# Kernel tuning notes

Hardware: AMD Instinct MI355X
Metric: run time of the kernel (lower is better)

## Reference

```python
import jax, jax.numpy as jnp
import numpy as np

ALPHA = 0.25
GAMMA = 2.0
LAMBDA_T = 0.1


def count_components(fg):
    """Count 6-connected components per volume. fg: [M,H,W,D] bool.
    Min-label propagation + pointer jumping (parallel union-find style CCL),
    matching scipy.ndimage.label's default face-connectivity structure.
    Returns float32 [M] component counts."""
    M, H, W, D = fg.shape
    N = H * W * D
    BIG = jnp.int32(N)  # sentinel label for background / padding
    idx = jnp.arange(N, dtype=jnp.int32).reshape(1, H, W, D)
    L0 = jnp.broadcast_to(idx, fg.shape)

    def shift(a, axis, d):
        # b[i] = a[i-d] along `axis`, padded with BIG outside the volume
        pad = [(0, 0)] * 4
        pad[axis] = (max(d, 0), max(-d, 0))
        ap = jnp.pad(a, pad, constant_values=N)
        sl = [slice(None)] * 4
        sl[axis] = slice(max(-d, 0), max(-d, 0) + a.shape[axis])
        return ap[tuple(sl)]

    def one_step(L):
        Lv = jnp.where(fg, L, BIG)
        m = Lv
        for ax in (1, 2, 3):
            for d in (1, -1):
                m = jnp.minimum(m, shift(Lv, ax, d))
        Ln = jnpp_min = jnp.where(fg, jnp.minimum(L, m), L)
        # pointer jumping (L <- L[L]) twice for log-depth convergence
        Lf = Ln.reshape(M, N)
        Lf = jnp.take_along_axis(Lf, Lf, axis=1)
        Lf = jnp.take_along_axis(Lf, Lf, axis=1)
        return Lf.reshape(M, H, W, D)

    def cond(s):
        return s[1]

    def body(s):
        L, _ = s
        Ln = one_step(L)
        return (Ln, jnp.any(Ln != L))

    L, _ = jax.lax.while_loop(cond, body, (L0, jnp.bool_(True)))
    # at fixed point every foreground component carries its min linear index;
    # roots satisfy L[i] == i
    roots = fg & (L == idx)
    return jnp.sum(roots, axis=(1, 2, 3)).astype(jnp.float32)


def _focal(x, t):
    p = jax.nn.sigmoid(x)
    pt = jnp.where(t == 1, p, 1.0 - p)
    bce = jax.nn.softplus(x) - x * t  # BCE-with-logits, elementwise
    alpha_t = jnp.where(t == 1, ALPHA, 1.0 - ALPHA)
    return jnp.mean(alpha_t * (1.0 - pt) ** GAMMA * bce)


def _topology(x, t):
    B, C = x.shape[:2]
    spatial = x.shape[2:]
    fg_p = (jax.nn.sigmoid(x) > 0.5).reshape(B * C, *spatial)
    fg_t = (t > 0.5).reshape(B * C, *spatial)
    cc_p = count_components(fg_p).reshape(B, C).mean(axis=0)  # mean over batch per class
    cc_t = count_components(fg_t).reshape(B, C).mean(axis=0)
    return jnp.mean(jnp.abs(cc_p - cc_t))  # sum over classes / C


def setup_inputs() -> dict:
    key = jax.random.key(0)
    k1, k2 = jax.random.split(key)
    shape = (2, 2, 96, 96, 96)
    pred_logits = jax.random.normal(k1, shape, dtype=jnp.float32)
    target_binary = jax.random.randint(k2, shape, 0, 2).astype(jnp.float32)
    return {"pred_logits": pred_logits, "target_binary": target_binary}


def reference(pred_logits, target_binary):
    focal = _focal(pred_logits, target_binary)
    topo = jax.lax.stop_gradient(_topology(pred_logits, target_binary))
    return focal + LAMBDA_T * topo
```

## Files before the change

kernel.cpp:

```cpp
#include <hip/hip_runtime.h>
#include <math.h>

#define N_VOX (96*96*96)
#define NVOL 8
#define NEL (4*N_VOX)
#define PLANE (96*96)

#define TW 8
#define TH 8
#define TILES_W 12
#define TILES_H 12
#define TILE_VOX (96*TW*TH)
#define TILE_WORDS (TILE_VOX/32)

#define NBPLANES 11
#define NPAIRS (2*NBPLANES)
#define FACES_PER_VOL (2*NPAIRS*PLANE)
#define MAXR 40192
#define FALLR 65536
#define SEGCAP 4608
#define HT2N 4096
#define MAX_PROBES 16

#define WS_ACC   0
#define WS_ROOT  256
#define WS_EVT   1536
#define WS_PCNT  2816
#define WS_HDR   4096

__device__ __forceinline__ int uf_find(int* __restrict__ L, int x) {
    int r = x;
    int p = L[r];
    while (p != r) { r = p; p = L[r]; }
    if (r != x) atomicMin(&L[x], r);
    return r;
}

__device__ __forceinline__ int uf_merge(int* __restrict__ L, int l1, int l2) {
    int ev = 0;
    while (l1 != l2) {
        if (l1 < l2) { int t = l1; l1 = l2; l2 = t; }
        int l3 = atomicMin(&L[l1], l2);
        if (l3 == l1) { ev++; l1 = l2; }
        else l1 = l3;
    }
    return ev;
}

__device__ __forceinline__ void merge_local(int* lab, int l1, int l2) {
    while (l1 != l2 && l1 != lab[l1]) l1 = lab[l1];
    while (l1 != l2 && l2 != lab[l2]) l2 = lab[l2];
    while (l1 != l2) {
        if (l1 < l2) { int t = l1; l1 = l2; l2 = t; }
        int l3 = atomicMin(&lab[l1], l2);
        l1 = (l3 == l1) ? l2 : l3;
    }
}

__device__ __forceinline__ int run_start(const unsigned* fm, int i, int d) {
    int rowb = (i - d) >> 5;
    int k = d >> 5, bit = d & 31;
    unsigned below = bit ? (~fm[rowb + k] & ((1u << bit) - 1)) : 0u;
    int z = -1;
    if (below) z = (k << 5) + 31 - __builtin_clz(below);
    else if (k > 0) {
        unsigned n1 = ~fm[rowb + k - 1];
        if (n1) z = ((k - 1) << 5) + 31 - __builtin_clz(n1);
        else if (k > 1) {
            unsigned n0 = ~fm[rowb];
            if (n0) z = 31 - __builtin_clz(n0);
        }
    }
    return (i - d) + z + 1;
}

__global__ __launch_bounds__(256) void ccl_local(const float* __restrict__ pred,
                                                 const float* __restrict__ targ,
                                                 unsigned short* __restrict__ faces,
                                                 int* __restrict__ rootcnt,
                                                 float* __restrict__ acc,
                                                 int vbase) {
    __shared__ int lab[TILE_VOX];
    __shared__ unsigned fm[TILE_WORDS];
    __shared__ float fws[4];
    __shared__ int   iws[4];
    __shared__ int   gbase;

    int vloc = blockIdx.y;
    int v = vbase + vloc;
    int tile = blockIdx.x;
    int tw = tile % TILES_W, th = tile / TILES_W;
    int w0 = tw * TW, h0 = th * TH;
    int tbase = h0 * PLANE + w0 * 96;
    unsigned short* Fw = faces + (size_t)vloc * FACES_PER_VOL;
    unsigned short* Fh = Fw + 2 * NBPLANES * PLANE;

    float fsum = 0.0f;
    for (int it = 0; it < TILE_VOX / 256; it++) {
        int i = it * 256 + threadIdx.x;
        int lh = i / 768;
        int j = tbase + i + lh * 8448;
        bool f;
        if (v < 4) {
            float xv = pred[(size_t)v * N_VOX + j];
            float tv = targ[(size_t)v * N_VOX + j];
            f = xv > 0.0f;
            float m   = (tv == 1.0f) ? -xv : xv;
            float at  = (tv == 1.0f) ? 0.25f : 0.75f;
            float e   = __expf(-fabsf(m));
            float inv = 1.0f / (1.0f + e);
            float sig = inv * ((m >= 0.0f) ? 1.0f : e);
            float sp  = fmaxf(m, 0.0f) + __logf(1.0f + e);
            fsum += at * sig * sig * sp;
        } else {
            f = targ[(size_t)(v - 4) * N_VOX + j] > 0.5f;
        }
        unsigned long long bal = __ballot(f);
        if ((threadIdx.x & 63) == 0) {
            fm[i >> 5]       = (unsigned)bal;
            fm[(i >> 5) + 1] = (unsigned)(bal >> 32);
        }
        lab[i] = i;
    }
    __syncthreads();

    for (int t = threadIdx.x; t < 336; t += 256) {
        bool wdir = t < 168;
        int tt = wdir ? t : t - 168;
        int lh, lw, k;
        if (wdir) { lh = tt / 21; int rem = tt % 21; lw = rem / 3; k = rem % 3; }
        else      { lh = tt / 24; int rem = tt % 24; lw = rem / 3; k = rem % 3; }
        int wb = (lh * 8 + lw) * 3 + k;
        int nb = wb + (wdir ? 3 : 24);
        unsigned ov = fm[wb] & fm[nb];
        if (!ov) continue;
        unsigned carry = (k > 0) ? ((fm[wb - 1] & fm[nb - 1]) >> 31) : 0u;
        unsigned starts = ov & ~((ov << 1) | carry);
        int base_i = wb << 5;
        int dir = wdir ? 96 : 768;
        while (starts) {
            int b = __builtin_ctz(starts);
            starts &= starts - 1;
            int i = base_i + b;
            int d = (k << 5) + b;
            merge_local(lab, run_start(fm, i, d), run_start(fm, i + dir, d));
        }
    }
    __syncthreads();

    int myroots = 0;
    for (int t = threadIdx.x; t < TILE_WORDS; t += 256) {
        unsigned m = fm[t];
        if (!m) continue;
        unsigned carry = (t % 3) ? (fm[t - 1] >> 31) : 0u;
        unsigned starts = m & ~((m << 1) | carry);
        int base_i = t << 5;
        while (starts) {
            int b = __builtin_ctz(starts); starts &= starts - 1;
            if (lab[base_i + b] == base_i + b) myroots++;
        }
    }
    int s = myroots;
    for (int off = 1; off < 64; off <<= 1) {
        int tv2 = __shfl_up(s, off, 64);
        if ((threadIdx.x & 63) >= off) s += tv2;
    }
    int wid = threadIdx.x >> 6;
    if ((threadIdx.x & 63) == 63) iws[wid] = s;
    __syncthreads();
    int wbase = 0;
    for (int k = 0; k < wid; k++) wbase += iws[k];
    if (threadIdx.x == 0)
        gbase = atomicAdd(&rootcnt[v << 5], iws[0] + iws[1] + iws[2] + iws[3]);
    __syncthreads();
    int nid = gbase + wbase + (s - myroots);

    for (int t = threadIdx.x; t < TILE_WORDS; t += 256) {
        unsigned m = fm[t];
        if (!m) continue;
        unsigned carry = (t % 3) ? (fm[t - 1] >> 31) : 0u;
        unsigned starts = m & ~((m << 1) | carry);
        int base_i = t << 5;
        while (starts) {
            int b = __builtin_ctz(starts); starts &= starts - 1;
            int i = base_i + b;
            if (lab[i] == i) lab[i] = ~(nid++);
        }
    }
    __syncthreads();

    for (int t = threadIdx.x; t < TILE_WORDS; t += 256) {
        unsigned m = fm[t];
        if (!m) continue;
        unsigned carry = (t % 3) ? (fm[t - 1] >> 31) : 0u;
        unsigned starts = m & ~((m << 1) | carry);
        int base_i = t << 5;
        while (starts) {
            int b = __builtin_ctz(starts); starts &= starts - 1;
            int i = base_i + b;
            int p = lab[i];
            if (p >= 0) {
                int r = p, q2 = lab[r];
                while (q2 >= 0) { r = q2; q2 = lab[r]; }
                lab[i] = q2;
            }
        }
    }
    __syncthreads();

    for (int t = threadIdx.x; t < 768; t += 256) {
        int f  = t / 192;
        int g  = t % 192;
        int u  = g / 24;
        int d4 = (g % 24) * 4;
        int i0; unsigned short* dst;
        if (f == 0) {
            if (tw == 0) continue;
            i0  = u * 768 + d4;
            dst = Fw + ((tw - 1) * 2 + 1) * PLANE + (h0 + u) * 96 + d4;
        } else if (f == 1) {
            if (tw == TILES_W - 1) continue;
            i0  = u * 768 + 7 * 96 + d4;
            dst = Fw + (tw * 2) * PLANE + (h0 + u) * 96 + d4;
        } else if (f == 2) {
            if (th == 0) continue;
            i0  = u * 96 + d4;
            dst = Fh + ((th - 1) * 2 + 1) * PLANE + (w0 + u) * 96 + d4;
        } else {
            if (th == TILES_H - 1) continue;
            i0  = 7 * 768 + u * 96 + d4;
            dst = Fh + (th * 2) * PLANE + (w0 + u) * 96 + d4;
        }
        unsigned mw = fm[i0 >> 5];
        unsigned short vals[4];
        bool prevf = false;
        for (int q = 0; q < 4; q++) {
            bool fb = (mw >> ((d4 & 31) + q)) & 1;
            if (fb) vals[q] = prevf ? vals[q - 1]
                                    : (unsigned short)(~lab[run_start(fm, i0 + q, d4 + q)]);
            else vals[q] = 0xFFFFu;
            prevf = fb;
        }
        *(ushort4*)dst = make_ushort4(vals[0], vals[1], vals[2], vals[3]);
    }

    for (int off = 32; off; off >>= 1) fsum += __shfl_down(fsum, off, 64);
    if ((threadIdx.x & 63) == 0) fws[wid] = fsum;
    __syncthreads();
    if (threadIdx.x == 0) {
        float ft = fws[0] + fws[1] + fws[2] + fws[3];
        if (v < 4 && ft != 0.0f) atomicAdd(acc, ft);
    }
}

__global__ __launch_bounds__(256) void ccl_pairs(const unsigned short* __restrict__ faces,
                                                 unsigned* __restrict__ pairs,
                                                 int* __restrict__ pcnt,
                                                 int vbase) {
    __shared__ unsigned ht[HT2N];
    __shared__ int nloc;
    for (int i = threadIdx.x; i < HT2N; i += 256) ht[i] = 0xFFFFFFFFu;
    if (threadIdx.x == 0) nloc = 0;
    __syncthreads();

    int f    = blockIdx.x;
    int vloc = blockIdx.y;
    int v    = vbase + vloc;
    const unsigned short* A = faces + (size_t)vloc * FACES_PER_VOL
                                    + (size_t)(2 * f) * PLANE;
    const unsigned short* B = A + PLANE;
    unsigned* pb = pairs + ((size_t)vloc * NPAIRS + f) * SEGCAP;

    const int GPP = PLANE / 8;
    for (int g = threadIdx.x; g < GPP; g += 256) {
        int e8 = g * 8;
        int4 aw = *(const int4*)(A + e8);
        int4 bw = *(const int4*)(B + e8);
        unsigned a32[4] = {(unsigned)aw.x, (unsigned)aw.y, (unsigned)aw.z, (unsigned)aw.w};
        unsigned b32[4] = {(unsigned)bw.x, (unsigned)bw.y, (unsigned)bw.z, (unsigned)bw.w};
        bool pf = false;
        if (e8 % 96) pf = (A[e8 - 1] != 0xFFFFu) && (B[e8 - 1] != 0xFFFFu);
        #pragma unroll
        for (int q = 0; q < 8; q++) {
            unsigned av = (a32[q >> 1] >> ((q & 1) * 16)) & 0xFFFFu;
            unsigned bv = (b32[q >> 1] >> ((q & 1) * 16)) & 0xFFFFu;
            bool f2 = (av != 0xFFFFu) && (bv != 0xFFFFu);
            if (f2 && !pf && av != bv) {
                unsigned lo = av < bv ? av : bv;
                unsigned hi = av < bv ? bv : av;
                unsigned key = (lo << 16) | hi;
                unsigned h = (key * 2654435761u) >> 20;
                bool fresh = false;
                for (int pr = 0; pr < MAX_PROBES; pr++) {
                    unsigned prev = atomicCAS(&ht[h], 0xFFFFFFFFu, key);
                    if (prev == 0xFFFFFFFFu) { fresh = true; break; }
                    if (prev == key) break;
                    h = (h + 1) & (HT2N - 1);
                    if (pr == MAX_PROBES - 1) fresh = true;
                }
                if (fresh) {
                    int ix = atomicAdd(&nloc, 1);
                    pb[ix] = key;
                }
            }
            pf = f2;
        }
    }
    __syncthreads();
    if (threadIdx.x == 0) pcnt[v * NPAIRS + f] = nloc;
}

__global__ __launch_bounds__(1024) void ccl_union(const unsigned* __restrict__ pairs,
                                                  int* __restrict__ gfall,
                                                  const int* __restrict__ rootcnt,
                                                  const int* __restrict__ pcnt,
                                                  int* __restrict__ events,
                                                  int vbase) {
    __shared__ int slab[MAXR];
    __shared__ int wsum[16];
    int vloc = blockIdx.x;
    int v = vbase + vloc;
    int R  = rootcnt[v << 5];

    int* lab = (R <= MAXR) ? (int*)slab : (gfall + (size_t)vloc * FALLR);
    for (int i = threadIdx.x; i < R; i += 1024) lab[i] = i;
    __syncthreads();

    int ev = 0;
    for (int f = 0; f < NPAIRS; f++) {
        int np = pcnt[v * NPAIRS + f];
        const unsigned* pb = pairs + ((size_t)vloc * NPAIRS + f) * SEGCAP;
        for (int i = threadIdx.x; i < np; i += 1024) {
            unsigned key = pb[i];
            int a = (int)(key >> 16), b = (int)(key & 0xFFFFu);
            int ra = uf_find(lab, a);
            int rb = uf_find(lab, b);
            if (ra != rb) ev += uf_merge(lab, ra, rb);
        }
    }

    for (int off = 32; off; off >>= 1) ev += __shfl_down(ev, off, 64);
    if ((threadIdx.x & 63) == 0) wsum[threadIdx.x >> 6] = ev;
    __syncthreads();
    if (threadIdx.x == 0) {
        int tot = 0;
        for (int k = 0; k < 16; k++) tot += wsum[k];
        events[v << 5] = tot;
    }
}

__global__ void finalize_kernel(const float* __restrict__ acc,
                                const int* __restrict__ rootcnt,
                                const int* __restrict__ events,
                                float* __restrict__ out) {
    float focal = acc[0] / (float)NEL;
    float c[NVOL];
    for (int v = 0; v < NVOL; v++)
        c[v] = (float)(rootcnt[v << 5] - events[v << 5]);
    float dp0 = 0.5f * (c[0] + c[2]);
    float dp1 = 0.5f * (c[1] + c[3]);
    float dt0 = 0.5f * (c[4] + c[6]);
    float dt1 = 0.5f * (c[5] + c[7]);
    float topo = 0.5f * (fabsf(dp0 - dt0) + fabsf(dp1 - dt1));
    out[0] = focal + 0.1f * topo;
}

extern "C" void kernel_launch(void* const* d_in, const int* in_sizes, int n_in,
                              void* d_out, int out_size, void* d_ws, size_t ws_size,
                              hipStream_t stream) {
    const float* pred = (const float*)d_in[0];
    const float* targ = (const float*)d_in[1];
    float* out = (float*)d_out;

    float* acc     = (float*)((char*)d_ws + WS_ACC);
    int*   rootcnt = (int*)((char*)d_ws + WS_ROOT);
    int*   events  = (int*)((char*)d_ws + WS_EVT);
    int*   pcnt    = (int*)((char*)d_ws + WS_PCNT);
    unsigned short* faces = (unsigned short*)((char*)d_ws + WS_HDR);

    size_t per_vol = (size_t)FACES_PER_VOL * 2
                   + (size_t)NPAIRS * SEGCAP * 4
                   + (size_t)FALLR * 4;
    size_t avail   = (ws_size > WS_HDR) ? ws_size - WS_HDR : 0;
    int vols_per_pass = (int)(avail / per_vol);
    if (vols_per_pass > NVOL) vols_per_pass = NVOL;
    if (vols_per_pass < 1) vols_per_pass = 1;
    unsigned* pairs = (unsigned*)(faces + (size_t)vols_per_pass * FACES_PER_VOL);
    int* gfall = (int*)(pairs + (size_t)vols_per_pass * NPAIRS * SEGCAP);

    hipMemsetAsync(d_ws, 0, WS_HDR, stream);

    for (int vbase = 0; vbase < NVOL; vbase += vols_per_pass) {
        int nv = NVOL - vbase;
        if (nv > vols_per_pass) nv = vols_per_pass;
        dim3 tgrid(TILES_W * TILES_H, nv);
        ccl_local<<<tgrid, dim3(256), 0, stream>>>(pred, targ, faces,
                                                   rootcnt, acc, vbase);
        dim3 pgrid(NPAIRS, nv);
        ccl_pairs<<<pgrid, dim3(256), 0, stream>>>(faces, pairs, pcnt, vbase);
        ccl_union<<<dim3(nv), dim3(1024), 0, stream>>>(pairs, gfall, rootcnt,
                                                       pcnt, events, vbase);
    }

    finalize_kernel<<<1, 1, 0, stream>>>(acc, rootcnt, events, out);
}
```

Before: 169.0 us.

## Label runs instead of voxels in local CCL using popcount run ranks

Switches the per-tile union-find in ccl_local from one label per voxel to one compact label per foreground run. A run index is found from a per-word prefix count of run starts plus a popcount. This replaces the run_start scans, the per-voxel label initialisation and the repeated bitmask walks in the root counting, renumbering and flattening passes with plain loops over run indices. It also halves the shared label array, which may raise occupancy. The cost is an extra block-wide prefix scan and two small shared arrays.

```diff
diff --git a/kernel.cpp b/kernel.cpp
--- a/kernel.cpp
+++ b/kernel.cpp
@@ -12,6 +12,7 @@
 #define TILES_H 12
 #define TILE_VOX (96*TW*TH)
 #define TILE_WORDS (TILE_VOX/32)
+#define MAXRUNS 3072
 
 #define NBPLANES 11
 #define NPAIRS (2*NBPLANES)
@@ -57,21 +58,11 @@
     }
 }
 
-__device__ __forceinline__ int run_start(const unsigned* fm, int i, int d) {
-    int rowb = (i - d) >> 5;
-    int k = d >> 5, bit = d & 31;
-    unsigned below = bit ? (~fm[rowb + k] & ((1u << bit) - 1)) : 0u;
-    int z = -1;
-    if (below) z = (k << 5) + 31 - __builtin_clz(below);
-    else if (k > 0) {
-        unsigned n1 = ~fm[rowb + k - 1];
-        if (n1) z = ((k - 1) << 5) + 31 - __builtin_clz(n1);
-        else if (k > 1) {
-            unsigned n0 = ~fm[rowb];
-            if (n0) z = 31 - __builtin_clz(n0);
-        }
-    }
-    return (i - d) + z + 1;
+__device__ __forceinline__ int rrank(const unsigned* __restrict__ sm,
+                                     const int* __restrict__ wpf, int i) {
+    int w = i >> 5, b = i & 31;
+    unsigned mask = (2u << b) - 1u;
+    return wpf[w] + __popc(sm[w] & mask) - 1;
 }
 
 __global__ __launch_bounds__(256) void ccl_local(const float* __restrict__ pred,
@@ -80,8 +71,10 @@
                                                  int* __restrict__ rootcnt,
                                                  float* __restrict__ acc,
                                                  int vbase) {
-    __shared__ int lab[TILE_VOX];
+    __shared__ int      lab[MAXRUNS];
     __shared__ unsigned fm[TILE_WORDS];
+    __shared__ unsigned sm[TILE_WORDS];
+    __shared__ int      wpf[TILE_WORDS];
     __shared__ float fws[4];
     __shared__ int   iws[4];
     __shared__ int   gbase;
@@ -120,52 +113,66 @@
             fm[i >> 5]       = (unsigned)bal;
             fm[(i >> 5) + 1] = (unsigned)(bal >> 32);
         }
-        lab[i] = i;
-    }
+    }
+    __syncthreads();
+
+    int cnt = 0;
+    {
+        unsigned st = 0;
+        if (threadIdx.x < TILE_WORDS) {
+            unsigned m = fm[threadIdx.x];
+            unsigned carry = (threadIdx.x % 3) ? (fm[threadIdx.x - 1] >> 31) : 0u;
+            st = m & ~((m << 1) | carry);
+            sm[threadIdx.x] = st;
+            cnt = __popc(st);
+        }
+    }
+    int inc = cnt;
+    for (int off = 1; off < 64; off <<= 1) {
+        int u = __shfl_up(inc, off, 64);
+        if ((threadIdx.x & 63) >= off) inc += u;
+    }
+    int wid = threadIdx.x >> 6;
+    if ((threadIdx.x & 63) == 63) iws[wid] = inc;
+    for (int r = threadIdx.x; r < MAXRUNS; r += 256) lab[r] = r;
+    __syncthreads();
+    int woff = 0;
+    for (int k = 0; k < wid; k++) woff += iws[k];
+    if (threadIdx.x < TILE_WORDS) wpf[threadIdx.x] = woff + inc - cnt;
+    int Nr = iws[0] + iws[1] + iws[2];
     __syncthreads();
 
     for (int t = threadIdx.x; t < 336; t += 256) {
-        bool wdir = t < 168;
-        int tt = wdir ? t : t - 168;
+        bool wdirn = t < 168;
+        int tt = wdirn ? t : t - 168;
         int lh, lw, k;
-        if (wdir) { lh = tt / 21; int rem = tt % 21; lw = rem / 3; k = rem % 3; }
-        else      { lh = tt / 24; int rem = tt % 24; lw = rem / 3; k = rem % 3; }
+        if (wdirn) { lh = tt / 21; int rem = tt % 21; lw = rem / 3; k = rem % 3; }
+        else       { lh = tt / 24; int rem = tt % 24; lw = rem / 3; k = rem % 3; }
         int wb = (lh * 8 + lw) * 3 + k;
-        int nb = wb + (wdir ? 3 : 24);
+        int nb = wb + (wdirn ? 3 : 24);
         unsigned ov = fm[wb] & fm[nb];
         if (!ov) continue;
         unsigned carry = (k > 0) ? ((fm[wb - 1] & fm[nb - 1]) >> 31) : 0u;
         unsigned starts = ov & ~((ov << 1) | carry);
         int base_i = wb << 5;
-        int dir = wdir ? 96 : 768;
+        int dir = wdirn ? 96 : 768;
         while (starts) {
             int b = __builtin_ctz(starts);
             starts &= starts - 1;
             int i = base_i + b;
-            int d = (k << 5) + b;
-            merge_local(lab, run_start(fm, i, d), run_start(fm, i + dir, d));
+            merge_local(lab, rrank(sm, wpf, i), rrank(sm, wpf, i + dir));
         }
     }
     __syncthreads();
 
     int myroots = 0;
-    for (int t = threadIdx.x; t < TILE_WORDS; t += 256) {
-        unsigned m = fm[t];
-        if (!m) continue;
-        unsigned carry = (t % 3) ? (fm[t - 1] >> 31) : 0u;
-        unsigned starts = m & ~((m << 1) | carry);
-        int base_i = t << 5;
-        while (starts) {
-            int b = __builtin_ctz(starts); starts &= starts - 1;
-            if (lab[base_i + b] == base_i + b) myroots++;
-        }
-    }
+    for (int r = threadIdx.x; r < Nr; r += 256)
+        if (lab[r] == r) myroots++;
     int s = myroots;
     for (int off = 1; off < 64; off <<= 1) {
-        int tv2 = __shfl_up(s, off, 64);
-        if ((threadIdx.x & 63) >= off) s += tv2;
-    }
-    int wid = threadIdx.x >> 6;
+        int u = __shfl_up(s, off, 64);
+        if ((threadIdx.x & 63) >= off) s += u;
+    }
     if ((threadIdx.x & 63) == 63) iws[wid] = s;
     __syncthreads();
     int wbase = 0;
@@ -174,36 +181,16 @@
         gbase = atomicAdd(&rootcnt[v << 5], iws[0] + iws[1] + iws[2] + iws[3]);
     __syncthreads();
     int nid = gbase + wbase + (s - myroots);
-
-    for (int t = threadIdx.x; t < TILE_WORDS; t += 256) {
-        unsigned m = fm[t];
-        if (!m) continue;
-        unsigned carry = (t % 3) ? (fm[t - 1] >> 31) : 0u;
-        unsigned starts = m & ~((m << 1) | carry);
-        int base_i = t << 5;
-        while (starts) {
-            int b = __builtin_ctz(starts); starts &= starts - 1;
-            int i = base_i + b;
-            if (lab[i] == i) lab[i] = ~(nid++);
-        }
-    }
-    __syncthreads();
-
-    for (int t = threadIdx.x; t < TILE_WORDS; t += 256) {
-        unsigned m = fm[t];
-        if (!m) continue;
-        unsigned carry = (t % 3) ? (fm[t - 1] >> 31) : 0u;
-        unsigned starts = m & ~((m << 1) | carry);
-        int base_i = t << 5;
-        while (starts) {
-            int b = __builtin_ctz(starts); starts &= starts - 1;
-            int i = base_i + b;
-            int p = lab[i];
-            if (p >= 0) {
-                int r = p, q2 = lab[r];
-                while (q2 >= 0) { r = q2; q2 = lab[r]; }
-                lab[i] = q2;
-            }
+    for (int r = threadIdx.x; r < Nr; r += 256)
+        if (lab[r] == r) lab[r] = ~(nid++);
+    __syncthreads();
+
+    for (int r = threadIdx.x; r < Nr; r += 256) {
+        int p = lab[r];
+        if (p >= 0) {
+            int q2 = lab[p];
+            while (q2 >= 0) { p = q2; q2 = lab[p]; }
+            lab[r] = q2;
         }
     }
     __syncthreads();
@@ -237,7 +224,7 @@
         for (int q = 0; q < 4; q++) {
             bool fb = (mw >> ((d4 & 31) + q)) & 1;
             if (fb) vals[q] = prevf ? vals[q - 1]
-                                    : (unsigned short)(~lab[run_start(fm, i0 + q, d4 + q)]);
+                                    : (unsigned short)(~lab[rrank(sm, wpf, i0 + q)]);
             else vals[q] = 0xFFFFu;
             prevf = fb;
         }
```

New measurement: 162.1 us. -4.1%, faster.
